# Optimization experiments

Hardware: AMD Instinct MI355X
Metric: run time of the kernel (lower is better)

Reference implementation:

```python
import jax, jax.numpy as jnp
import numpy as np

N_SEQ, N_RES, C_M, C_Z, C, N_HEAD = 256, 256, 256, 128, 32, 8
EPS = 1e-5


def layernorm(x, w, b):
    mu = jnp.mean(x, axis=-1, keepdims=True)
    var = jnp.mean((x - mu) ** 2, axis=-1, keepdims=True)
    return (x - mu) * jax.lax.rsqrt(var + EPS) * w + b


def setup_inputs() -> dict:
    key = jax.random.key(0)
    ks = jax.random.split(key, 12)
    s = 0.02
    return {
        "m": jax.random.normal(ks[0], (N_SEQ, N_RES, C_M), jnp.float32),
        "z": jax.random.normal(ks[1], (N_RES, N_RES, C_Z), jnp.float32),
        "ln_m_w": jnp.ones((C_M,), jnp.float32),
        "ln_m_b": jnp.zeros((C_M,), jnp.float32),
        "ln_z_w": jnp.ones((C_Z,), jnp.float32),
        "ln_z_b": jnp.zeros((C_Z,), jnp.float32),
        "Wz": jax.random.normal(ks[2], (C_Z, N_HEAD), jnp.float32) * s,   # pair bias proj, no bias
        "Wq": jax.random.normal(ks[3], (C_M, N_HEAD * C), jnp.float32) * s,
        "Wk": jax.random.normal(ks[4], (C_M, N_HEAD * C), jnp.float32) * s,
        "Wv": jax.random.normal(ks[5], (C_M, N_HEAD * C), jnp.float32) * s,
        "Wg": jax.random.normal(ks[6], (C_M, N_HEAD * C), jnp.float32) * s,
        "bg": jnp.zeros((N_HEAD * C,), jnp.float32),
        "Wo": jax.random.normal(ks[7], (N_HEAD * C, C_M), jnp.float32) * s,
        "bo": jnp.zeros((C_M,), jnp.float32),
    }


def reference(m, z, ln_m_w, ln_m_b, ln_z_w, ln_z_b, Wz, Wq, Wk, Wv, Wg, bg, Wo, bo):
    # LayerNorm on msa and pair reps
    mn = layernorm(m, ln_m_w, ln_m_b)                       # (S, R, c_m)
    b = layernorm(z, ln_z_w, ln_z_b) @ Wz                    # (R, R, H)
    b = jnp.moveaxis(b, -1, -3)                              # (H, R, R)

    def proj(W):  # (S, R, H, C) -> (S, H, R, C)
        return (mn @ W).reshape(N_SEQ, N_RES, N_HEAD, C).transpose(0, 2, 1, 3)

    q = proj(Wq) / jnp.sqrt(jnp.float32(C))
    k = proj(Wk)
    v = proj(Wv)

    scores = jnp.einsum("shqc,shkc->shqk", q, k) + b         # bias broadcasts over S
    a = jax.nn.softmax(scores, axis=-1)
    o = jnp.einsum("shqk,shkc->shqc", a, v)                  # (S, H, R, C)
    o = o.transpose(0, 2, 1, 3).reshape(N_SEQ, N_RES, N_HEAD * C)

    g = jax.nn.sigmoid(mn @ Wg + bg)                          # gating
    return (g * o) @ Wo + bo                                  # (S, R, c_m)
```

## Files before the change

### kernel.cpp

```cpp
#include <hip/hip_runtime.h>
#include <stdint.h>

#define NSEQ 256
#define NRES 256
#define CM   256
#define CZ   128
#define CH   32
#define NHEAD 8
#define EPSF 1e-5f

typedef __bf16 bf16x8 __attribute__((ext_vector_type(8)));
typedef float  f32x4  __attribute__((ext_vector_type(4)));
typedef float  f32x16 __attribute__((ext_vector_type(16)));

__device__ __forceinline__ ushort f2bf(float f) {
    union { float f; uint32_t u; } v; v.f = f;
    uint32_t r = (v.u + 0x7FFFu + ((v.u >> 16) & 1u)) >> 16;
    return (ushort)r;
}
__device__ __forceinline__ float bf2f(ushort h) {
    union { uint32_t u; float f; } v; v.u = ((uint32_t)h) << 16;
    return v.f;
}
__device__ __forceinline__ float bfl(uint32_t u) {
    union { uint32_t x; float f; } v; v.x = u << 16; return v.f;
}
__device__ __forceinline__ float bfh(uint32_t u) {
    union { uint32_t x; float f; } v; v.x = u & 0xffff0000u; return v.f;
}
__device__ __forceinline__ unsigned int cvt_pk_bf16(float lo, float hi_) {
    unsigned int r;
    asm("v_cvt_pk_bf16_f32 %0, %1, %2" : "=v"(r) : "v"(lo), "v"(hi_));
    return r;
}

__device__ __forceinline__ void gload16(const void* g, void* l) {
    __builtin_amdgcn_global_load_lds(
        (const __attribute__((address_space(1))) void*)g,
        (__attribute__((address_space(3))) void*)l,
        16, 0, 0);
}

__global__ __launch_bounds__(256) void pre_kernel(const float* __restrict__ m,
                                                  const float* __restrict__ ln_m_w,
                                                  const float* __restrict__ ln_m_b,
                                                  const float* __restrict__ z,
                                                  const float* __restrict__ ln_z_w,
                                                  const float* __restrict__ ln_z_b,
                                                  const float* __restrict__ Wz,
                                                  const float* __restrict__ Wq,
                                                  const float* __restrict__ Wk,
                                                  const float* __restrict__ Wv,
                                                  const float* __restrict__ Wg,
                                                  const float* __restrict__ Wo,
                                                  ushort* __restrict__ mn,
                                                  ushort* __restrict__ biasb,
                                                  ushort* __restrict__ Wt,
                                                  ushort* __restrict__ WoT) {
    int b = blockIdx.x;
    int t = threadIdx.x;
    int lane = t & 63;

    if (b < 16384) {
        int gw = (b * 256 + t) >> 6;
        const float* row = m + (size_t)gw * 256;
        float4 x = *(const float4*)(row + lane * 4);
        float s  = x.x + x.y + x.z + x.w;
        float sq = x.x * x.x + x.y * x.y + x.z * x.z + x.w * x.w;
#pragma unroll
        for (int off = 32; off; off >>= 1) {
            s  += __shfl_xor(s, off, 64);
            sq += __shfl_xor(sq, off, 64);
        }
        float mu  = s * (1.0f / 256.0f);
        float var = sq * (1.0f / 256.0f) - mu * mu;
        float rs  = rsqrtf(var + EPSF);
        float4 wv = *(const float4*)(ln_m_w + lane * 4);
        float4 bv = *(const float4*)(ln_m_b + lane * 4);
        ushort4 o;
        o.x = f2bf((x.x - mu) * rs * wv.x + bv.x);
        o.y = f2bf((x.y - mu) * rs * wv.y + bv.y);
        o.z = f2bf((x.z - mu) * rs * wv.z + bv.z);
        o.w = f2bf((x.w - mu) * rs * wv.w + bv.w);
        *(ushort4*)(mn + (size_t)gw * 256 + lane * 4) = o;
    } else if (b < 18432) {
        int gw = ((b - 16384) * 256 + t) >> 6;
        float wz0[8], wz1[8];
#pragma unroll
        for (int h = 0; h < 8; ++h) {
            wz0[h] = Wz[(2 * lane) * 8 + h];
            wz1[h] = Wz[(2 * lane + 1) * 8 + h];
        }
        float w0 = ln_z_w[2 * lane], w1 = ln_z_w[2 * lane + 1];
        float b0 = ln_z_b[2 * lane], b1 = ln_z_b[2 * lane + 1];
        for (int row = gw; row < 65536; row += 8192) {
            float2 x = *(const float2*)(z + (size_t)row * 128 + 2 * lane);
            float s = x.x + x.y, sq = x.x * x.x + x.y * x.y;
#pragma unroll
            for (int off = 32; off; off >>= 1) {
                s  += __shfl_xor(s, off, 64);
                sq += __shfl_xor(sq, off, 64);
            }
            float mu = s * (1.0f / 128.0f);
            float rs = rsqrtf(sq * (1.0f / 128.0f) - mu * mu + EPSF);
            float z0 = (x.x - mu) * rs * w0 + b0;
            float z1 = (x.y - mu) * rs * w1 + b1;
            float acc[8];
#pragma unroll
            for (int h = 0; h < 8; ++h) acc[h] = z0 * wz0[h] + z1 * wz1[h];
            float u[4];
#pragma unroll
            for (int i = 0; i < 4; ++i) {
                float send = (lane & 1) ? acc[i] : acc[i + 4];
                float rec  = __shfl_xor(send, 1, 64);
                u[i] = ((lane & 1) ? acc[i + 4] : acc[i]) + rec;
            }
            float v2[2];
#pragma unroll
            for (int i = 0; i < 2; ++i) {
                float send = (lane & 2) ? u[i] : u[i + 2];
                float rec  = __shfl_xor(send, 2, 64);
                v2[i] = ((lane & 2) ? u[i + 2] : u[i]) + rec;
            }
            float send = (lane & 4) ? v2[0] : v2[1];
            float rec  = __shfl_xor(send, 4, 64);
            float vv = ((lane & 4) ? v2[1] : v2[0]) + rec;
            vv += __shfl_xor(vv, 8, 64);
            vv += __shfl_xor(vv, 16, 64);
            vv += __shfl_xor(vv, 32, 64);
            if (lane < 8) {
                int hh = ((lane & 1) << 2) | (lane & 2) | ((lane >> 2) & 1);
                int jc = row & 31;
                int posv = ((jc & 4) << 2) | ((jc & 24) >> 1) | (jc & 3);
                biasb[hh * 65536 + (row & ~31) + posv] = f2bf(vv);
            }
        }
    } else {
        int n = b - 18432;
        int k = t;
        if (n < 1024) {
            int nn = n & 255;
            const float* src;
            float scale = 1.0f;
            if      (n < 256) { src = Wq; scale = 0.17677669529663687f; }
            else if (n < 512) { src = Wk; }
            else if (n < 768) { src = Wv; }
            else              { src = Wg; }
            Wt[n * 256 + k] = f2bf(src[k * 256 + nn] * scale);
        } else {
            int nn = n - 1024;
            WoT[nn * 256 + k] = f2bf(Wo[k * 256 + nn]);
        }
    }
}

__global__ __launch_bounds__(256, 4) void proj_gemm_kernel(const ushort* __restrict__ mn,
                                                           const ushort* __restrict__ Wt,
                                                           const float* __restrict__ bg,
                                                           ushort* __restrict__ Q,
                                                           ushort* __restrict__ K,
                                                           ushort* __restrict__ Vt,
                                                           ushort* __restrict__ G) {
    __shared__ ushort SH[16384];
    int bid = blockIdx.x;
    int wid = ((bid & 7) << 9) | (bid >> 3);
    int by = wid >> 3, bx = wid & 7;
    int m0 = by << 7, n0 = bx << 7;
    int t = threadIdx.x, lane = t & 63, w = t >> 6;
    int l15 = lane & 15, l4 = lane >> 4;
    int wr = w >> 1, wc = w & 1;

    int srow  = t >> 2;
    int sgran = t & 3;
    int scol  = (sgran ^ ((srow >> 1) & 3)) << 3;
    const ushort* Ag = mn + (size_t)(m0 + srow) * 256 + scol;
    const ushort* Bg = Wt + (size_t)(n0 + srow) * 256 + scol;

    auto stage = [&](int kt) {
        int k0 = kt << 5;
        int bufo = (kt & 1) << 13;
        gload16(Ag + k0,             &SH[bufo + t * 8]);
        gload16(Ag + 64 * 256 + k0,  &SH[bufo + 2048 + t * 8]);
        gload16(Bg + k0,             &SH[bufo + 4096 + t * 8]);
        gload16(Bg + 64 * 256 + k0,  &SH[bufo + 4096 + 2048 + t * 8]);
    };

    f32x4 acc[4][4] = {};
    stage(0);

    int rg = (l4 ^ ((l15 >> 1) & 3)) << 3;

    for (int kt = 0; kt < 8; ++kt) {
        __syncthreads();
        if (kt < 7) stage(kt + 1);
        int bufo = (kt & 1) << 13;
        bf16x8 af[4], bfr[4];
#pragma unroll
        for (int mi = 0; mi < 4; ++mi) {
            int row = wr * 64 + mi * 16 + l15;
            af[mi] = *(const bf16x8*)&SH[bufo + row * 32 + rg];
        }
#pragma unroll
        for (int ni = 0; ni < 4; ++ni) {
            int row = wc * 64 + ni * 16 + l15;
            bfr[ni] = *(const bf16x8*)&SH[bufo + 4096 + row * 32 + rg];
        }
#pragma unroll
        for (int mi = 0; mi < 4; ++mi)
#pragma unroll
            for (int ni = 0; ni < 4; ++ni)
                acc[mi][ni] = __builtin_amdgcn_mfma_f32_16x16x32_bf16(af[mi], bfr[ni], acc[mi][ni], 0, 0, 0);
    }

    __syncthreads();

    int region = bx >> 1;
    int ss = m0 >> 8;

    if (region == 2) {
        int rbase = (m0 & 255) + wr * 64 + l4 * 4;
#pragma unroll
        for (int ni = 0; ni < 4; ++ni) {
            int nn = (n0 & 255) + wc * 64 + ni * 16 + l15;
            int h = nn >> 5, c = nn & 31;
#pragma unroll
            for (int mi = 0; mi < 4; ++mi) {
                int rr = rbase + mi * 16;
                ushort4 pv;
                pv.x = f2bf(acc[mi][ni][0]); pv.y = f2bf(acc[mi][ni][1]);
                pv.z = f2bf(acc[mi][ni][2]); pv.w = f2bf(acc[mi][ni][3]);
                *(ushort4*)&Vt[((size_t)(ss * 8 + h) * 32 + c) * 256 + rr] = pv;
            }
        }
    } else {
        ushort* E = SH + w * 1152;
        int base_nn = (bx & 1) * 128 + wc * 64;
        int rloc = lane >> 2, seg = lane & 3;
#pragma unroll
        for (int mi = 0; mi < 4; ++mi) {
            if (region == 3) {
#pragma unroll
                for (int ni = 0; ni < 4; ++ni) {
                    float bgv = bg[base_nn + ni * 16 + l15];
#pragma unroll
                    for (int r = 0; r < 4; ++r) {
                        float x = acc[mi][ni][r] + bgv;
                        E[(l4 * 4 + r) * 72 + ni * 16 + l15] =
                            f2bf(1.0f / (1.0f + __expf(-x)));
                    }
                }
            } else {
#pragma unroll
                for (int ni = 0; ni < 4; ++ni)
#pragma unroll
                    for (int r = 0; r < 4; ++r)
                        E[(l4 * 4 + r) * 72 + ni * 16 + l15] = f2bf(acc[mi][ni][r]);
            }
            uint4 v0 = *(const uint4*)&E[rloc * 72 + seg * 16];
            uint4 v1 = *(const uint4*)&E[rloc * 72 + seg * 16 + 8];
            int rr  = (m0 & 255) + wr * 64 + mi * 16 + rloc;
            int nn0 = base_nn + seg * 16;
            int h0 = nn0 >> 5, c0 = nn0 & 31;
            int nn1 = nn0 + 8;
            int h1 = nn1 >> 5, c1 = nn1 & 31;
            if (region <= 1) {
                ushort* dst = (region == 0) ? Q : K;
                *(uint4*)&dst[(size_t)(ss * 8 + h0) * 8192 + rr * 32 + c0] = v0;
                *(uint4*)&dst[(size_t)(ss * 8 + h1) * 8192 + rr * 32 + c1] = v1;
            } else {
                *(uint4*)&G[((size_t)h0 << 21) + (ss << 13) + (rr << 5) + c0] = v0;
                *(uint4*)&G[((size_t)h1 << 21) + (ss << 13) + (rr << 5) + c1] = v1;
            }
        }
    }
}

__global__ __launch_bounds__(512, 4) void attn_kernel(const ushort* __restrict__ Q,
                                                      const ushort* __restrict__ K,
                                                      const ushort* __restrict__ Vt,
                                                      const ushort* __restrict__ G,
                                                      const ushort* __restrict__ biasb,
                                                      ushort* __restrict__ GO) {
    __shared__ ushort smem[32768];
    const int t = threadIdx.x;
    const int lane = t & 63, w = t >> 6;
    const int l31 = lane & 31, hi = lane >> 5;
    const int h = blockIdx.x & 7, s0 = blockIdx.x >> 3;
    const int q0 = w * 32;

    auto stage = [&](int i) {
        size_t shb = (size_t)((i * 64 + s0) * 8 + h) * 8192;
        const ushort* Kg = K + shb;
        const ushort* Vg = Vt + shb;
        int bufo = (i & 1) * 16384;
#pragma unroll
        for (int rd = 0; rd < 2; ++rd) {
            int g1 = rd * 512 + t;
            int kk = g1 >> 2;
            int lgk = (g1 & 3) ^ ((kk >> 1) & 3);
            gload16(Kg + kk * 32 + lgk * 8, &smem[bufo + g1 * 8]);
            int cc = g1 >> 5;
            int lgv = (g1 & 31) ^ (cc & 7);
            gload16(Vg + cc * 256 + lgv * 8, &smem[bufo + 8192 + g1 * 8]);
        }
    };

    stage(0);

    for (int i = 0; i < 4; ++i) {
        __syncthreads();
        if (i < 3) stage(i + 1);

        const int s = i * 64 + s0;
        const size_t shb = (size_t)(s * 8 + h) * 8192;
        const int bufo = (i & 1) * 16384;

        bf16x8 qf0 = *(const bf16x8*)&Q[shb + (size_t)(q0 + l31) * 32 + hi * 8];
        bf16x8 qf1 = *(const bf16x8*)&Q[shb + (size_t)(q0 + l31) * 32 + 16 + hi * 8];

        const ushort* bp = biasb + (size_t)h * 65536 + (size_t)(q0 + l31) * 256 + hi * 16;
        const int vbase = bufo + 8192 + l31 * 256;
        const int vswz = l31 & 7;

        float l_run = 0.f;
        f32x16 oa = {}, ob = {};

#pragma unroll 2
        for (int kt = 0; kt < 8; ++kt) {
            uint4 b0 = *(const uint4*)&bp[kt * 32];
            uint4 b1 = *(const uint4*)&bp[kt * 32 + 8];
            f32x16 sa;
            sa[0]  = bfl(b0.x); sa[1]  = bfh(b0.x);
            sa[2]  = bfl(b0.y); sa[3]  = bfh(b0.y);
            sa[4]  = bfl(b0.z); sa[5]  = bfh(b0.z);
            sa[6]  = bfl(b0.w); sa[7]  = bfh(b0.w);
            sa[8]  = bfl(b1.x); sa[9]  = bfh(b1.x);
            sa[10] = bfl(b1.y); sa[11] = bfh(b1.y);
            sa[12] = bfl(b1.z); sa[13] = bfh(b1.z);
            sa[14] = bfl(b1.w); sa[15] = bfh(b1.w);

            int krow = kt * 32 + l31;
            int swz = (krow >> 1) & 3;
            int rb = bufo + krow * 32;
            bf16x8 kf0 = *(const bf16x8*)&smem[rb + ((hi ^ swz) << 3)];
            bf16x8 kf1 = *(const bf16x8*)&smem[rb + (((2 + hi) ^ swz) << 3)];
            sa = __builtin_amdgcn_mfma_f32_32x32x16_bf16(kf0, qf0, sa, 0, 0, 0);
            sa = __builtin_amdgcn_mfma_f32_32x32x16_bf16(kf1, qf1, sa, 0, 0, 0);

            float ls0 = 0.f, ls1 = 0.f;
#pragma unroll
            for (int r = 0; r < 16; r += 2) {
                float p0 = __expf(sa[r]);
                float p1 = __expf(sa[r + 1]);
                sa[r] = p0; sa[r + 1] = p1;
                ls0 += p0; ls1 += p1;
            }
            l_run += ls0 + ls1;

            unsigned int w0[4], w1[4];
#pragma unroll
            for (int mm = 0; mm < 4; ++mm) {
                w0[mm] = cvt_pk_bf16(sa[4 * mm + 0], sa[4 * mm + 1]);
                w1[mm] = cvt_pk_bf16(sa[4 * mm + 2], sa[4 * mm + 3]);
            }
#pragma unroll
            for (int hh = 0; hh < 2; ++hh) {
                unsigned int F0 = w0[2 * hh], H0 = w0[2 * hh + 1];
                unsigned int F1 = w1[2 * hh], H1 = w1[2 * hh + 1];
                asm("v_permlane32_swap_b32 %0, %1" : "+v"(F0), "+v"(H0));
                asm("v_permlane32_swap_b32 %0, %1" : "+v"(F1), "+v"(H1));
                uint4 fw = make_uint4(F0, F1, H0, H1);
                bf16x8 pf = *(bf16x8*)&fw;
                int g = kt * 4 + hh * 2 + hi;
                bf16x8 vf = *(const bf16x8*)&smem[vbase + ((g ^ vswz) << 3)];
                if (hh) ob = __builtin_amdgcn_mfma_f32_32x32x16_bf16(vf, pf, ob, 0, 0, 0);
                else    oa = __builtin_amdgcn_mfma_f32_32x32x16_bf16(vf, pf, oa, 0, 0, 0);
            }
        }

        l_run += __shfl_xor(l_run, 32, 64);
        float rinv = 1.0f / l_run;

        const size_t grow = ((size_t)h << 21) + ((size_t)s << 13) + ((q0 + l31) << 5) + hi * 4;
#pragma unroll
        for (int g = 0; g < 4; ++g) {
            ushort4 gv = *(const ushort4*)&G[grow + g * 8];
            float o0 = (oa[4 * g + 0] + ob[4 * g + 0]) * rinv * bf2f(gv.x);
            float o1 = (oa[4 * g + 1] + ob[4 * g + 1]) * rinv * bf2f(gv.y);
            float o2 = (oa[4 * g + 2] + ob[4 * g + 2]) * rinv * bf2f(gv.z);
            float o3 = (oa[4 * g + 3] + ob[4 * g + 3]) * rinv * bf2f(gv.w);
            ushort4 ov;
            ov.x = f2bf(o0); ov.y = f2bf(o1); ov.z = f2bf(o2); ov.w = f2bf(o3);
            *(ushort4*)&GO[grow + g * 8] = ov;
        }
    }
}

__global__ __launch_bounds__(256) void out_gemm_kernel(const ushort* __restrict__ GO,
                                                       const ushort* __restrict__ WoT,
                                                       const float* __restrict__ bo,
                                                       float* __restrict__ out) {
    __shared__ ushort SH[32768];
    int bid = blockIdx.x;
    int wid = ((bid & 7) << 7) | (bid >> 3);
    int by = wid >> 1, bx = wid & 1;
    int m0 = by << 7, n0 = bx << 7;
    int t = threadIdx.x, lane = t & 63, w = t >> 6;
    int l15 = lane & 15, l4 = lane >> 4;
    int wr = w >> 1, wc = w & 1;

    int srow  = t >> 3;
    int scolh = (((lane & 7) ^ ((lane >> 3) & 7)) << 3);
    const ushort* Ag = GO + ((size_t)(scolh >> 5) << 21) + ((size_t)(m0 + srow) << 5) + (scolh & 31);
    const ushort* Bg = WoT + (size_t)(n0 + srow) * 256 + scolh;

    auto stage = [&](int kt) {
        int k0 = kt << 6;
        int bufo = (kt & 1) << 14;
#pragma unroll
        for (int i = 0; i < 4; ++i) {
            gload16(Ag + ((size_t)kt << 22) + (i << 10), &SH[bufo + t * 8 + i * 2048]);
            gload16(Bg + (size_t)(i * 32) * 256 + k0, &SH[bufo + 8192 + t * 8 + i * 2048]);
        }
    };

    f32x4 acc[4][4] = {};
    stage(0);

    for (int kt = 0; kt < 4; ++kt) {
        __syncthreads();
        if (kt < 3) stage(kt + 1);
        int bufo = (kt & 1) << 14;
#pragma unroll
        for (int ks = 0; ks < 2; ++ks) {
            int xr = ks * 4 + l4;
            bf16x8 af[4], bfr[4];
#pragma unroll
            for (int mi = 0; mi < 4; ++mi) {
                int row = wr * 64 + mi * 16 + l15;
                af[mi] = *(const bf16x8*)&SH[bufo + row * 64 + ((xr ^ (l15 & 7)) << 3)];
            }
#pragma unroll
            for (int ni = 0; ni < 4; ++ni) {
                int row = wc * 64 + ni * 16 + l15;
                bfr[ni] = *(const bf16x8*)&SH[bufo + 8192 + row * 64 + ((xr ^ (l15 & 7)) << 3)];
            }
#pragma unroll
            for (int mi = 0; mi < 4; ++mi)
#pragma unroll
                for (int ni = 0; ni < 4; ++ni)
                    acc[mi][ni] = __builtin_amdgcn_mfma_f32_16x16x32_bf16(af[mi], bfr[ni], acc[mi][ni], 0, 0, 0);
        }
    }

    int crow0 = m0 + wr * 64 + l4 * 4;
#pragma unroll
    for (int ni = 0; ni < 4; ++ni) {
        int col = n0 + wc * 64 + ni * 16 + l15;
        float bov = bo[col];
#pragma unroll
        for (int mi = 0; mi < 4; ++mi)
#pragma unroll
            for (int r = 0; r < 4; ++r)
                out[(size_t)(crow0 + mi * 16 + r) * 256 + col] = acc[mi][ni][r] + bov;
    }
}

extern "C" void kernel_launch(void* const* d_in, const int* in_sizes, int n_in,
                              void* d_out, int out_size, void* d_ws, size_t ws_size,
                              hipStream_t stream) {
    const float* m      = (const float*)d_in[0];
    const float* z      = (const float*)d_in[1];
    const float* ln_m_w = (const float*)d_in[2];
    const float* ln_m_b = (const float*)d_in[3];
    const float* ln_z_w = (const float*)d_in[4];
    const float* ln_z_b = (const float*)d_in[5];
    const float* Wz     = (const float*)d_in[6];
    const float* Wq     = (const float*)d_in[7];
    const float* Wk     = (const float*)d_in[8];
    const float* Wv     = (const float*)d_in[9];
    const float* Wg     = (const float*)d_in[10];
    const float* bg     = (const float*)d_in[11];
    const float* Wo     = (const float*)d_in[12];
    const float* bo     = (const float*)d_in[13];
    float* out = (float*)d_out;

    char* ws = (char*)d_ws;
    ushort* Wt    = (ushort*)(ws + 0);
    ushort* WoT   = (ushort*)(ws + 524288);
    ushort* biasb = (ushort*)(ws + 655360);
    ushort* mn    = (ushort*)(ws + 2752512);
    ushort* GO    = mn;
    ushort* Q     = (ushort*)(ws + 36306944);
    ushort* K     = (ushort*)(ws + 69861376);
    ushort* Vt    = (ushort*)(ws + 103415808);
    ushort* G     = (ushort*)(ws + 136970240);

    pre_kernel<<<19712, 256, 0, stream>>>(m, ln_m_w, ln_m_b, z, ln_z_w, ln_z_b,
                                          Wz, Wq, Wk, Wv, Wg, Wo,
                                          mn, biasb, Wt, WoT);
    proj_gemm_kernel<<<4096, 256, 0, stream>>>(mn, Wt, bg, Q, K, Vt, G);
    attn_kernel<<<512, 512, 0, stream>>>(Q, K, Vt, G, biasb, GO);
    out_gemm_kernel<<<1024, 256, 0, stream>>>(GO, WoT, bo, out);
}
```

Baseline: 190.0 us.

## Fuse QKVG projection into attention kernel, keeping per-head Q/K/V in LDS

Replaces the separate projection GEMM and attention kernels with one kernel per (sequence, head). Each block loads its normalized MSA rows, computes that head's K, V, Q and gate slices with MFMA, and stages them in LDS. Attention then runs directly from LDS, removing the large Q/K/Vt/G round trips through global memory and one kernel launch. In exchange, the weight slices and mn rows are re-read once per head, there is no LDS pipelining, and register pressure rises because the mn slab and the gate values stay resident.

```diff
diff --git a/kernel.cpp b/kernel.cpp
--- a/kernel.cpp
+++ b/kernel.cpp
@@ -18,9 +18,8 @@
     uint32_t r = (v.u + 0x7FFFu + ((v.u >> 16) & 1u)) >> 16;
     return (ushort)r;
 }
-__device__ __forceinline__ float bf2f(ushort h) {
-    union { uint32_t u; float f; } v; v.u = ((uint32_t)h) << 16;
-    return v.f;
+__device__ __forceinline__ uint32_t pack_bf16_rne(float lo, float hi_) {
+    return (uint32_t)f2bf(lo) | ((uint32_t)f2bf(hi_) << 16);
 }
 __device__ __forceinline__ float bfl(uint32_t u) {
     union { uint32_t x; float f; } v; v.x = u << 16; return v.f;
@@ -32,13 +31,6 @@
     unsigned int r;
     asm("v_cvt_pk_bf16_f32 %0, %1, %2" : "=v"(r) : "v"(lo), "v"(hi_));
     return r;
-}
-
-__device__ __forceinline__ void gload16(const void* g, void* l) {
-    __builtin_amdgcn_global_load_lds(
-        (const __attribute__((address_space(1))) void*)g,
-        (__attribute__((address_space(3))) void*)l,
-        16, 0, 0);
 }
 
 __global__ __launch_bounds__(256) void pre_kernel(const float* __restrict__ m,
@@ -154,245 +146,162 @@
     }
 }
 
-__global__ __launch_bounds__(256, 4) void proj_gemm_kernel(const ushort* __restrict__ mn,
-                                                           const ushort* __restrict__ Wt,
-                                                           const float* __restrict__ bg,
-                                                           ushort* __restrict__ Q,
-                                                           ushort* __restrict__ K,
-                                                           ushort* __restrict__ Vt,
-                                                           ushort* __restrict__ G) {
-    __shared__ ushort SH[16384];
-    int bid = blockIdx.x;
-    int wid = ((bid & 7) << 9) | (bid >> 3);
-    int by = wid >> 3, bx = wid & 7;
-    int m0 = by << 7, n0 = bx << 7;
-    int t = threadIdx.x, lane = t & 63, w = t >> 6;
-    int l15 = lane & 15, l4 = lane >> 4;
-    int wr = w >> 1, wc = w & 1;
-
-    int srow  = t >> 2;
-    int sgran = t & 3;
-    int scol  = (sgran ^ ((srow >> 1) & 3)) << 3;
-    const ushort* Ag = mn + (size_t)(m0 + srow) * 256 + scol;
-    const ushort* Bg = Wt + (size_t)(n0 + srow) * 256 + scol;
-
-    auto stage = [&](int kt) {
-        int k0 = kt << 5;
-        int bufo = (kt & 1) << 13;
-        gload16(Ag + k0,             &SH[bufo + t * 8]);
-        gload16(Ag + 64 * 256 + k0,  &SH[bufo + 2048 + t * 8]);
-        gload16(Bg + k0,             &SH[bufo + 4096 + t * 8]);
-        gload16(Bg + 64 * 256 + k0,  &SH[bufo + 4096 + 2048 + t * 8]);
-    };
-
-    f32x4 acc[4][4] = {};
-    stage(0);
-
-    int rg = (l4 ^ ((l15 >> 1) & 3)) << 3;
-
-    for (int kt = 0; kt < 8; ++kt) {
-        __syncthreads();
-        if (kt < 7) stage(kt + 1);
-        int bufo = (kt & 1) << 13;
-        bf16x8 af[4], bfr[4];
-#pragma unroll
-        for (int mi = 0; mi < 4; ++mi) {
-            int row = wr * 64 + mi * 16 + l15;
-            af[mi] = *(const bf16x8*)&SH[bufo + row * 32 + rg];
-        }
-#pragma unroll
-        for (int ni = 0; ni < 4; ++ni) {
-            int row = wc * 64 + ni * 16 + l15;
-            bfr[ni] = *(const bf16x8*)&SH[bufo + 4096 + row * 32 + rg];
-        }
-#pragma unroll
-        for (int mi = 0; mi < 4; ++mi)
-#pragma unroll
-            for (int ni = 0; ni < 4; ++ni)
-                acc[mi][ni] = __builtin_amdgcn_mfma_f32_16x16x32_bf16(af[mi], bfr[ni], acc[mi][ni], 0, 0, 0);
-    }
-
-    __syncthreads();
-
-    int region = bx >> 1;
-    int ss = m0 >> 8;
-
-    if (region == 2) {
-        int rbase = (m0 & 255) + wr * 64 + l4 * 4;
-#pragma unroll
-        for (int ni = 0; ni < 4; ++ni) {
-            int nn = (n0 & 255) + wc * 64 + ni * 16 + l15;
-            int h = nn >> 5, c = nn & 31;
-#pragma unroll
-            for (int mi = 0; mi < 4; ++mi) {
-                int rr = rbase + mi * 16;
-                ushort4 pv;
-                pv.x = f2bf(acc[mi][ni][0]); pv.y = f2bf(acc[mi][ni][1]);
-                pv.z = f2bf(acc[mi][ni][2]); pv.w = f2bf(acc[mi][ni][3]);
-                *(ushort4*)&Vt[((size_t)(ss * 8 + h) * 32 + c) * 256 + rr] = pv;
-            }
-        }
-    } else {
-        ushort* E = SH + w * 1152;
-        int base_nn = (bx & 1) * 128 + wc * 64;
-        int rloc = lane >> 2, seg = lane & 3;
-#pragma unroll
-        for (int mi = 0; mi < 4; ++mi) {
-            if (region == 3) {
-#pragma unroll
-                for (int ni = 0; ni < 4; ++ni) {
-                    float bgv = bg[base_nn + ni * 16 + l15];
-#pragma unroll
-                    for (int r = 0; r < 4; ++r) {
-                        float x = acc[mi][ni][r] + bgv;
-                        E[(l4 * 4 + r) * 72 + ni * 16 + l15] =
-                            f2bf(1.0f / (1.0f + __expf(-x)));
-                    }
-                }
-            } else {
-#pragma unroll
-                for (int ni = 0; ni < 4; ++ni)
-#pragma unroll
-                    for (int r = 0; r < 4; ++r)
-                        E[(l4 * 4 + r) * 72 + ni * 16 + l15] = f2bf(acc[mi][ni][r]);
-            }
-            uint4 v0 = *(const uint4*)&E[rloc * 72 + seg * 16];
-            uint4 v1 = *(const uint4*)&E[rloc * 72 + seg * 16 + 8];
-            int rr  = (m0 & 255) + wr * 64 + mi * 16 + rloc;
-            int nn0 = base_nn + seg * 16;
-            int h0 = nn0 >> 5, c0 = nn0 & 31;
-            int nn1 = nn0 + 8;
-            int h1 = nn1 >> 5, c1 = nn1 & 31;
-            if (region <= 1) {
-                ushort* dst = (region == 0) ? Q : K;
-                *(uint4*)&dst[(size_t)(ss * 8 + h0) * 8192 + rr * 32 + c0] = v0;
-                *(uint4*)&dst[(size_t)(ss * 8 + h1) * 8192 + rr * 32 + c1] = v1;
-            } else {
-                *(uint4*)&G[((size_t)h0 << 21) + (ss << 13) + (rr << 5) + c0] = v0;
-                *(uint4*)&G[((size_t)h1 << 21) + (ss << 13) + (rr << 5) + c1] = v1;
-            }
-        }
-    }
-}
-
-__global__ __launch_bounds__(512, 4) void attn_kernel(const ushort* __restrict__ Q,
-                                                      const ushort* __restrict__ K,
-                                                      const ushort* __restrict__ Vt,
-                                                      const ushort* __restrict__ G,
-                                                      const ushort* __restrict__ biasb,
-                                                      ushort* __restrict__ GO) {
-    __shared__ ushort smem[32768];
+__global__ __launch_bounds__(512, 4) void fused_kernel(const ushort* __restrict__ mn,
+                                                       const ushort* __restrict__ Wt,
+                                                       const float* __restrict__ bg,
+                                                       const ushort* __restrict__ biasb,
+                                                       ushort* __restrict__ GO) {
+    __shared__ ushort smem[28928];
     const int t = threadIdx.x;
     const int lane = t & 63, w = t >> 6;
     const int l31 = lane & 31, hi = lane >> 5;
-    const int h = blockIdx.x & 7, s0 = blockIdx.x >> 3;
-    const int q0 = w * 32;
-
-    auto stage = [&](int i) {
-        size_t shb = (size_t)((i * 64 + s0) * 8 + h) * 8192;
-        const ushort* Kg = K + shb;
-        const ushort* Vg = Vt + shb;
-        int bufo = (i & 1) * 16384;
-#pragma unroll
-        for (int rd = 0; rd < 2; ++rd) {
-            int g1 = rd * 512 + t;
-            int kk = g1 >> 2;
-            int lgk = (g1 & 3) ^ ((kk >> 1) & 3);
-            gload16(Kg + kk * 32 + lgk * 8, &smem[bufo + g1 * 8]);
-            int cc = g1 >> 5;
-            int lgv = (g1 & 31) ^ (cc & 7);
-            gload16(Vg + cc * 256 + lgv * 8, &smem[bufo + 8192 + g1 * 8]);
-        }
-    };
-
-    stage(0);
-
-    for (int i = 0; i < 4; ++i) {
-        __syncthreads();
-        if (i < 3) stage(i + 1);
-
-        const int s = i * 64 + s0;
-        const size_t shb = (size_t)(s * 8 + h) * 8192;
-        const int bufo = (i & 1) * 16384;
-
-        bf16x8 qf0 = *(const bf16x8*)&Q[shb + (size_t)(q0 + l31) * 32 + hi * 8];
-        bf16x8 qf1 = *(const bf16x8*)&Q[shb + (size_t)(q0 + l31) * 32 + 16 + hi * 8];
-
-        const ushort* bp = biasb + (size_t)h * 65536 + (size_t)(q0 + l31) * 256 + hi * 16;
-        const int vbase = bufo + 8192 + l31 * 256;
-        const int vswz = l31 & 7;
-
-        float l_run = 0.f;
-        f32x16 oa = {}, ob = {};
+    const int h = blockIdx.x & 7, s = blockIdx.x >> 3;
+
+    const ushort* mrow = mn + ((size_t)(s * 256 + w * 32 + l31)) * 256 + hi * 8;
+    bf16x8 slab[16];
+#pragma unroll
+    for (int k2 = 0; k2 < 16; ++k2) slab[k2] = *(const bf16x8*)&mrow[k2 * 16];
+
+    const size_t wrow = (size_t)(h * 32 + l31) * 256 + hi * 8;
+
+    {
+        const ushort* wk = Wt + 256 * 256 + wrow;
+        f32x16 d = {};
+#pragma unroll
+        for (int k2 = 0; k2 < 16; ++k2)
+            d = __builtin_amdgcn_mfma_f32_32x32x16_bf16(*(const bf16x8*)&wk[k2 * 16], slab[k2], d, 0, 0, 0);
+        int krow = w * 32 + l31;
+#pragma unroll
+        for (int g = 0; g < 4; ++g) {
+            uint2 pr;
+            pr.x = pack_bf16_rne(d[4 * g + 0], d[4 * g + 1]);
+            pr.y = pack_bf16_rne(d[4 * g + 2], d[4 * g + 3]);
+            *(uint2*)&smem[krow * 40 + g * 8 + hi * 4] = pr;
+        }
+    }
+
+    {
+        const ushort* wv = Wt + 512 * 256 + wrow;
+        f32x16 d = {};
+#pragma unroll
+        for (int k2 = 0; k2 < 16; ++k2)
+            d = __builtin_amdgcn_mfma_f32_32x32x16_bf16(slab[k2], *(const bf16x8*)&wv[k2 * 16], d, 0, 0, 0);
+#pragma unroll
+        for (int g = 0; g < 4; ++g) {
+            uint2 pr;
+            pr.x = pack_bf16_rne(d[4 * g + 0], d[4 * g + 1]);
+            pr.y = pack_bf16_rne(d[4 * g + 2], d[4 * g + 3]);
+            *(uint2*)&smem[10240 + l31 * 264 + w * 32 + g * 8 + hi * 4] = pr;
+        }
+    }
+
+    {
+        const ushort* wq = Wt + wrow;
+        f32x16 d = {};
+#pragma unroll
+        for (int k2 = 0; k2 < 16; ++k2)
+            d = __builtin_amdgcn_mfma_f32_32x32x16_bf16(*(const bf16x8*)&wq[k2 * 16], slab[k2], d, 0, 0, 0);
+        ushort* Qp = &smem[18688 + w * 1280 + l31 * 40];
+#pragma unroll
+        for (int g = 0; g < 4; ++g) {
+            uint2 pr;
+            pr.x = pack_bf16_rne(d[4 * g + 0], d[4 * g + 1]);
+            pr.y = pack_bf16_rne(d[4 * g + 2], d[4 * g + 3]);
+            *(uint2*)&Qp[g * 8 + hi * 4] = pr;
+        }
+    }
+
+    f32x16 gval;
+    {
+        const ushort* wg = Wt + 768 * 256 + wrow;
+        f32x16 d = {};
+#pragma unroll
+        for (int k2 = 0; k2 < 16; ++k2)
+            d = __builtin_amdgcn_mfma_f32_32x32x16_bf16(*(const bf16x8*)&wg[k2 * 16], slab[k2], d, 0, 0, 0);
+#pragma unroll
+        for (int g = 0; g < 4; ++g) {
+            float4 b4 = *(const float4*)&bg[h * 32 + 8 * g + 4 * hi];
+            gval[4 * g + 0] = 1.0f / (1.0f + __expf(-(d[4 * g + 0] + b4.x)));
+            gval[4 * g + 1] = 1.0f / (1.0f + __expf(-(d[4 * g + 1] + b4.y)));
+            gval[4 * g + 2] = 1.0f / (1.0f + __expf(-(d[4 * g + 2] + b4.z)));
+            gval[4 * g + 3] = 1.0f / (1.0f + __expf(-(d[4 * g + 3] + b4.w)));
+        }
+    }
+
+    __syncthreads();
+
+    const ushort* Qp = &smem[18688 + w * 1280 + l31 * 40];
+    bf16x8 qf0 = *(const bf16x8*)&Qp[hi * 8];
+    bf16x8 qf1 = *(const bf16x8*)&Qp[16 + hi * 8];
+
+    const ushort* bp = biasb + (size_t)h * 65536 + (size_t)(w * 32 + l31) * 256 + hi * 16;
+
+    float l_run = 0.f;
+    f32x16 oa = {}, ob = {};
 
 #pragma unroll 2
-        for (int kt = 0; kt < 8; ++kt) {
-            uint4 b0 = *(const uint4*)&bp[kt * 32];
-            uint4 b1 = *(const uint4*)&bp[kt * 32 + 8];
-            f32x16 sa;
-            sa[0]  = bfl(b0.x); sa[1]  = bfh(b0.x);
-            sa[2]  = bfl(b0.y); sa[3]  = bfh(b0.y);
-            sa[4]  = bfl(b0.z); sa[5]  = bfh(b0.z);
-            sa[6]  = bfl(b0.w); sa[7]  = bfh(b0.w);
-            sa[8]  = bfl(b1.x); sa[9]  = bfh(b1.x);
-            sa[10] = bfl(b1.y); sa[11] = bfh(b1.y);
-            sa[12] = bfl(b1.z); sa[13] = bfh(b1.z);
-            sa[14] = bfl(b1.w); sa[15] = bfh(b1.w);
-
-            int krow = kt * 32 + l31;
-            int swz = (krow >> 1) & 3;
-            int rb = bufo + krow * 32;
-            bf16x8 kf0 = *(const bf16x8*)&smem[rb + ((hi ^ swz) << 3)];
-            bf16x8 kf1 = *(const bf16x8*)&smem[rb + (((2 + hi) ^ swz) << 3)];
-            sa = __builtin_amdgcn_mfma_f32_32x32x16_bf16(kf0, qf0, sa, 0, 0, 0);
-            sa = __builtin_amdgcn_mfma_f32_32x32x16_bf16(kf1, qf1, sa, 0, 0, 0);
-
-            float ls0 = 0.f, ls1 = 0.f;
-#pragma unroll
-            for (int r = 0; r < 16; r += 2) {
-                float p0 = __expf(sa[r]);
-                float p1 = __expf(sa[r + 1]);
-                sa[r] = p0; sa[r + 1] = p1;
-                ls0 += p0; ls1 += p1;
-            }
-            l_run += ls0 + ls1;
-
-            unsigned int w0[4], w1[4];
-#pragma unroll
-            for (int mm = 0; mm < 4; ++mm) {
-                w0[mm] = cvt_pk_bf16(sa[4 * mm + 0], sa[4 * mm + 1]);
-                w1[mm] = cvt_pk_bf16(sa[4 * mm + 2], sa[4 * mm + 3]);
-            }
-#pragma unroll
-            for (int hh = 0; hh < 2; ++hh) {
-                unsigned int F0 = w0[2 * hh], H0 = w0[2 * hh + 1];
-                unsigned int F1 = w1[2 * hh], H1 = w1[2 * hh + 1];
-                asm("v_permlane32_swap_b32 %0, %1" : "+v"(F0), "+v"(H0));
-                asm("v_permlane32_swap_b32 %0, %1" : "+v"(F1), "+v"(H1));
-                uint4 fw = make_uint4(F0, F1, H0, H1);
-                bf16x8 pf = *(bf16x8*)&fw;
-                int g = kt * 4 + hh * 2 + hi;
-                bf16x8 vf = *(const bf16x8*)&smem[vbase + ((g ^ vswz) << 3)];
-                if (hh) ob = __builtin_amdgcn_mfma_f32_32x32x16_bf16(vf, pf, ob, 0, 0, 0);
-                else    oa = __builtin_amdgcn_mfma_f32_32x32x16_bf16(vf, pf, oa, 0, 0, 0);
-            }
-        }
-
-        l_run += __shfl_xor(l_run, 32, 64);
-        float rinv = 1.0f / l_run;
-
-        const size_t grow = ((size_t)h << 21) + ((size_t)s << 13) + ((q0 + l31) << 5) + hi * 4;
-#pragma unroll
-        for (int g = 0; g < 4; ++g) {
-            ushort4 gv = *(const ushort4*)&G[grow + g * 8];
-            float o0 = (oa[4 * g + 0] + ob[4 * g + 0]) * rinv * bf2f(gv.x);
-            float o1 = (oa[4 * g + 1] + ob[4 * g + 1]) * rinv * bf2f(gv.y);
-            float o2 = (oa[4 * g + 2] + ob[4 * g + 2]) * rinv * bf2f(gv.z);
-            float o3 = (oa[4 * g + 3] + ob[4 * g + 3]) * rinv * bf2f(gv.w);
-            ushort4 ov;
-            ov.x = f2bf(o0); ov.y = f2bf(o1); ov.z = f2bf(o2); ov.w = f2bf(o3);
-            *(ushort4*)&GO[grow + g * 8] = ov;
-        }
+    for (int kt = 0; kt < 8; ++kt) {
+        uint4 b0 = *(const uint4*)&bp[kt * 32];
+        uint4 b1 = *(const uint4*)&bp[kt * 32 + 8];
+        f32x16 sa;
+        sa[0]  = bfl(b0.x); sa[1]  = bfh(b0.x);
+        sa[2]  = bfl(b0.y); sa[3]  = bfh(b0.y);
+        sa[4]  = bfl(b0.z); sa[5]  = bfh(b0.z);
+        sa[6]  = bfl(b0.w); sa[7]  = bfh(b0.w);
+        sa[8]  = bfl(b1.x); sa[9]  = bfh(b1.x);
+        sa[10] = bfl(b1.y); sa[11] = bfh(b1.y);
+        sa[12] = bfl(b1.z); sa[13] = bfh(b1.z);
+        sa[14] = bfl(b1.w); sa[15] = bfh(b1.w);
+
+        int rb = (kt * 32 + l31) * 40;
+        bf16x8 kf0 = *(const bf16x8*)&smem[rb + hi * 8];
+        bf16x8 kf1 = *(const bf16x8*)&smem[rb + 16 + hi * 8];
+        sa = __builtin_amdgcn_mfma_f32_32x32x16_bf16(kf0, qf0, sa, 0, 0, 0);
+        sa = __builtin_amdgcn_mfma_f32_32x32x16_bf16(kf1, qf1, sa, 0, 0, 0);
+
+        float ls0 = 0.f, ls1 = 0.f;
+#pragma unroll
+        for (int r = 0; r < 16; r += 2) {
+            float p0 = __expf(sa[r]);
+            float p1 = __expf(sa[r + 1]);
+            sa[r] = p0; sa[r + 1] = p1;
+            ls0 += p0; ls1 += p1;
+        }
+        l_run += ls0 + ls1;
+
+        unsigned int w0[4], w1[4];
+#pragma unroll
+        for (int mm = 0; mm < 4; ++mm) {
+            w0[mm] = cvt_pk_bf16(sa[4 * mm + 0], sa[4 * mm + 1]);
+            w1[mm] = cvt_pk_bf16(sa[4 * mm + 2], sa[4 * mm + 3]);
+        }
+#pragma unroll
+        for (int hh = 0; hh < 2; ++hh) {
+            unsigned int F0 = w0[2 * hh], H0 = w0[2 * hh + 1];
+            unsigned int F1 = w1[2 * hh], H1 = w1[2 * hh + 1];
+            asm("v_permlane32_swap_b32 %0, %1" : "+v"(F0), "+v"(H0));
+            asm("v_permlane32_swap_b32 %0, %1" : "+v"(F1), "+v"(H1));
+            uint4 fw = make_uint4(F0, F1, H0, H1);
+            bf16x8 pf = *(bf16x8*)&fw;
+            bf16x8 vf = *(const bf16x8*)&smem[10240 + l31 * 264 + kt * 32 + hh * 16 + hi * 8];
+            if (hh) ob = __builtin_amdgcn_mfma_f32_32x32x16_bf16(vf, pf, ob, 0, 0, 0);
+            else    oa = __builtin_amdgcn_mfma_f32_32x32x16_bf16(vf, pf, oa, 0, 0, 0);
+        }
+    }
+
+    l_run += __shfl_xor(l_run, 32, 64);
+    float rinv = 1.0f / l_run;
+
+    const size_t grow = ((size_t)h << 21) + ((size_t)s << 13) + ((size_t)(w * 32 + l31) << 5) + hi * 4;
+#pragma unroll
+    for (int g = 0; g < 4; ++g) {
+        float o0 = (oa[4 * g + 0] + ob[4 * g + 0]) * rinv * gval[4 * g + 0];
+        float o1 = (oa[4 * g + 1] + ob[4 * g + 1]) * rinv * gval[4 * g + 1];
+        float o2 = (oa[4 * g + 2] + ob[4 * g + 2]) * rinv * gval[4 * g + 2];
+        float o3 = (oa[4 * g + 3] + ob[4 * g + 3]) * rinv * gval[4 * g + 3];
+        ushort4 ov;
+        ov.x = f2bf(o0); ov.y = f2bf(o1); ov.z = f2bf(o2); ov.w = f2bf(o3);
+        *(ushort4*)&GO[grow + g * 8] = ov;
     }
 }
 
@@ -419,8 +328,12 @@
         int bufo = (kt & 1) << 14;
 #pragma unroll
         for (int i = 0; i < 4; ++i) {
-            gload16(Ag + ((size_t)kt << 22) + (i << 10), &SH[bufo + t * 8 + i * 2048]);
-            gload16(Bg + (size_t)(i * 32) * 256 + k0, &SH[bufo + 8192 + t * 8 + i * 2048]);
+            __builtin_amdgcn_global_load_lds(
+                (const __attribute__((address_space(1))) void*)(Ag + ((size_t)kt << 22) + (i << 10)),
+                (__attribute__((address_space(3))) void*)&SH[bufo + t * 8 + i * 2048], 16, 0, 0);
+            __builtin_amdgcn_global_load_lds(
+                (const __attribute__((address_space(1))) void*)(Bg + (size_t)(i * 32) * 256 + k0),
+                (__attribute__((address_space(3))) void*)&SH[bufo + 8192 + t * 8 + i * 2048], 16, 0, 0);
         }
     };
 
@@ -490,16 +403,11 @@
     ushort* WoT   = (ushort*)(ws + 524288);
     ushort* biasb = (ushort*)(ws + 655360);
     ushort* mn    = (ushort*)(ws + 2752512);
-    ushort* GO    = mn;
-    ushort* Q     = (ushort*)(ws + 36306944);
-    ushort* K     = (ushort*)(ws + 69861376);
-    ushort* Vt    = (ushort*)(ws + 103415808);
-    ushort* G     = (ushort*)(ws + 136970240);
+    ushort* GO    = (ushort*)(ws + 36306944);
 
     pre_kernel<<<19712, 256, 0, stream>>>(m, ln_m_w, ln_m_b, z, ln_z_w, ln_z_b,
                                           Wz, Wq, Wk, Wv, Wg, Wo,
                                           mn, biasb, Wt, WoT);
-    proj_gemm_kernel<<<4096, 256, 0, stream>>>(mn, Wt, bg, Q, K, Vt, G);
-    attn_kernel<<<512, 512, 0, stream>>>(Q, K, Vt, G, biasb, GO);
+    fused_kernel<<<2048, 512, 0, stream>>>(mn, Wt, bg, biasb, GO);
     out_gemm_kernel<<<1024, 256, 0, stream>>>(GO, WoT, bo, out);
 }
```

Result: slower. 262.6 us (+38.2%).
